# Performance work log

Hardware: AMD Instinct MI355X
Metric: run time of the kernel (lower is better)

Reference implementation:

```python
import jax, jax.numpy as jnp
import numpy as np

D_MODEL = 512
D_STATE = 16
D_CONV = 4
D_INNER = 1024  # expand_factor * d_model
HEADS = 8
D_K = D_MODEL // HEADS
EPS = 1e-5


def layer_norm(x, g, b):
    mu = jnp.mean(x, axis=-1, keepdims=True)
    var = jnp.var(x, axis=-1, keepdims=True)
    return (x - mu) / jnp.sqrt(var + EPS) * g + b


def silu(x):
    return x * jax.nn.sigmoid(x)


def setup_inputs() -> dict:
    key = jax.random.key(0)
    ks = jax.random.split(key, 20)
    s = 0.02

    def n(k, shape):
        return jax.random.normal(k, shape, jnp.float32) * s

    inp = {
        "x": jax.random.normal(ks[0], (8, 1024, D_MODEL), jnp.float32),
        # Mamba params (Linear weights stored as [in, out])
        "in_proj_w": n(ks[1], (D_MODEL, 2 * D_INNER)),
        "conv_w": n(ks[2], (D_INNER, D_CONV)),
        "conv_b": jnp.zeros((D_INNER,), jnp.float32),
        "x_proj_w": n(ks[3], (D_INNER, 2 * D_STATE)),
        "dt_proj_w": n(ks[4], (D_INNER, D_INNER)),
        "dt_proj_b": jnp.zeros((D_INNER,), jnp.float32),
        "A_log": jnp.log(jnp.arange(1, D_STATE + 1, dtype=jnp.float32)),
        "D": jnp.ones((D_INNER,), jnp.float32),
        "out_proj_w": n(ks[5], (D_INNER, D_MODEL)),
        # attention
        "wq_w": n(ks[6], (D_MODEL, D_MODEL)), "wq_b": jnp.zeros((D_MODEL,), jnp.float32),
        "wk_w": n(ks[7], (D_MODEL, D_MODEL)), "wk_b": jnp.zeros((D_MODEL,), jnp.float32),
        "wv_w": n(ks[8], (D_MODEL, D_MODEL)), "wv_b": jnp.zeros((D_MODEL,), jnp.float32),
        "wo_w": n(ks[9], (D_MODEL, D_MODEL)), "wo_b": jnp.zeros((D_MODEL,), jnp.float32),
        "attn_ln_g": jnp.ones((D_MODEL,), jnp.float32), "attn_ln_b": jnp.zeros((D_MODEL,), jnp.float32),
        # FFN
        "ffn_w1": n(ks[10], (D_MODEL, 4 * D_MODEL)), "ffn_b1": jnp.zeros((4 * D_MODEL,), jnp.float32),
        "ffn_w2": n(ks[11], (4 * D_MODEL, D_MODEL)), "ffn_b2": jnp.zeros((D_MODEL,), jnp.float32),
        # norms
        "norm1_g": jnp.ones((D_MODEL,), jnp.float32), "norm1_b": jnp.zeros((D_MODEL,), jnp.float32),
        "norm2_g": jnp.ones((D_MODEL,), jnp.float32), "norm2_b": jnp.zeros((D_MODEL,), jnp.float32),
        "norm3_g": jnp.ones((D_MODEL,), jnp.float32), "norm3_b": jnp.zeros((D_MODEL,), jnp.float32),
        # gate
        "gate_w": n(ks[12], (2 * D_MODEL, D_MODEL)), "gate_b": jnp.zeros((D_MODEL,), jnp.float32),
    }
    return inp


def selective_scan(u, delta, A, B, C, Dp):
    # u, delta: [b, L, d_inner]; B, C: [b, L, d_state]; A: [d_state]; Dp: [d_inner]
    def step(h, inp):
        u_i, d_i, B_i, C_i = inp
        dA = jnp.exp(d_i[:, None, :] * A[None, :, None])        # [b, S, di]
        h = h * dA + (d_i[:, None, :] * B_i[:, :, None]) * u_i[:, None, :]
        y_i = jnp.sum(h * C_i[:, :, None], axis=1)              # [b, di]
        return h, y_i

    b = u.shape[0]
    h0 = jnp.zeros((b, A.shape[0], u.shape[-1]), u.dtype)
    xs = (u.transpose(1, 0, 2), delta.transpose(1, 0, 2),
          B.transpose(1, 0, 2), C.transpose(1, 0, 2))
    _, ys = jax.lax.scan(step, h0, xs)                          # [L, b, di]
    y = ys.transpose(1, 0, 2)
    return y + u * Dp


def mamba(x, in_proj_w, conv_w, conv_b, x_proj_w, dt_proj_w, dt_proj_b, A_log, Dp, out_proj_w):
    L = x.shape[1]
    xr = x @ in_proj_w
    xm, res = jnp.split(xr, 2, axis=-1)                         # [b, L, di] each
    # causal depthwise conv1d: left pad d_conv-1
    xp = jnp.pad(xm, ((0, 0), (D_CONV - 1, 0), (0, 0)))
    xc = sum(conv_w[:, k] * xp[:, k:k + L, :] for k in range(D_CONV)) + conv_b
    xc = silu(xc)
    BC = xc @ x_proj_w
    B, C = jnp.split(BC, 2, axis=-1)                            # [b, L, d_state]
    delta = jax.nn.softplus(xc @ dt_proj_w + dt_proj_b)
    A = -jnp.exp(A_log)
    y = selective_scan(xc, delta, A, B, C, Dp)
    y = y * silu(res)
    return y @ out_proj_w


def attention(q_in, wq_w, wq_b, wk_w, wk_b, wv_w, wv_b, wo_w, wo_b, ln_g, ln_b):
    b, S, _ = q_in.shape
    Q = (q_in @ wq_w + wq_b).reshape(b, S, HEADS, D_K)
    K = (q_in @ wk_w + wk_b).reshape(b, S, HEADS, D_K)
    V = (q_in @ wv_w + wv_b).reshape(b, S, HEADS, D_K)
    scores = jnp.einsum('bqhd,bkhd->bhqk', Q, K) / np.sqrt(D_K).astype(np.float32)
    w = jax.nn.softmax(scores, axis=-1)
    out = jnp.einsum('bhqk,bkhd->bqhd', w, V).reshape(b, S, D_MODEL)
    out = out @ wo_w + wo_b
    return layer_norm(out + q_in, ln_g, ln_b), w


def reference(x, in_proj_w, conv_w, conv_b, x_proj_w, dt_proj_w, dt_proj_b, A_log, D,
              out_proj_w, wq_w, wq_b, wk_w, wk_b, wv_w, wv_b, wo_w, wo_b,
              attn_ln_g, attn_ln_b, ffn_w1, ffn_b1, ffn_w2, ffn_b2,
              norm1_g, norm1_b, norm2_g, norm2_b, norm3_g, norm3_b, gate_w, gate_b):
    mamba_out = mamba(layer_norm(x, norm1_g, norm1_b), in_proj_w, conv_w, conv_b,
                      x_proj_w, dt_proj_w, dt_proj_b, A_log, D, out_proj_w)
    x = x + mamba_out
    xn = layer_norm(x, norm2_g, norm2_b)
    attn_out, attn_w = attention(xn, wq_w, wq_b, wk_w, wk_b, wv_w, wv_b, wo_w, wo_b,
                                 attn_ln_g, attn_ln_b)
    x = x + attn_out
    combined = jnp.concatenate([mamba_out, attn_out], axis=-1)
    g = jax.nn.sigmoid(combined @ gate_w + gate_b)
    fused = g * mamba_out + (1.0 - g) * attn_out
    x = x + fused
    xn3 = layer_norm(x, norm3_g, norm3_b)
    ffn = jax.nn.gelu(xn3 @ ffn_w1 + ffn_b1) @ ffn_w2 + ffn_b2
    x = x + ffn
    return (x, attn_w)
```

## Files before the change

### kernel.cpp

```cpp
#include <hip/hip_runtime.h>

#define SEQL 1024
#define DMODEL 512
#define DINNER 1024
#define NROWS 8192
#define SEG 64
#define NSEG 16
#define LOG2E 1.4426950408889634f

typedef unsigned short u16;
typedef unsigned int u32;
using bf16x8 = __attribute__((ext_vector_type(8))) short;
using f32x4  = __attribute__((ext_vector_type(4))) float;
using u16x4  = __attribute__((ext_vector_type(4))) unsigned short;
using u16x8  = __attribute__((ext_vector_type(8))) unsigned short;

__device__ __forceinline__ float rcp_fast(float x){ return __builtin_amdgcn_rcpf(x); }
__device__ __forceinline__ float exp_fast(float x){ return __expf(x); }
#if __has_builtin(__builtin_amdgcn_exp2f)
__device__ __forceinline__ float exp2_fast(float x){ return __builtin_amdgcn_exp2f(x); }
#else
__device__ __forceinline__ float exp2_fast(float x){ return __expf(x*0.6931471805599453f); }
#endif
__device__ __forceinline__ float sigmoid_f(float x){ return rcp_fast(1.f+exp_fast(-x)); }
__device__ __forceinline__ float softplus_f(float x){ return fmaxf(x,0.f)+__logf(1.f+exp_fast(-fabsf(x))); }
__device__ __forceinline__ float gelu_f(float x){
  float u2 = 1.5957691216057308f*(x+0.044715f*x*x*x);
  float t = 1.f - 2.f*rcp_fast(1.f+exp_fast(u2));
  return 0.5f*x*(1.f+t);
}
__device__ __forceinline__ u16 f2bf(float f){
  u32 u = __builtin_bit_cast(u32, f);
  return (u16)((u + 0x7FFFu + ((u>>16)&1u)) >> 16);
}
__device__ __forceinline__ float bf2f(u16 h){
  return __builtin_bit_cast(float, (u32)h << 16);
}

typedef __attribute__((address_space(1))) const void g_void;
typedef __attribute__((address_space(3))) void l_void;
__device__ __forceinline__ void gl_lds16(const void* g, void* l){
  __builtin_amdgcn_global_load_lds((g_void*)g, (l_void*)l, 16, 0, 0);
}

struct WtDesc { const float* src; u16* dst; int K; int N; int t0; };
struct WtArgs { WtDesc d[11]; };

__global__ __launch_bounds__(256) void wt_k(WtArgs a)
{
  __shared__ float t[64][65];
  int bid = blockIdx.x;
  int i = 0;
  #pragma unroll
  for (int j=1;j<11;++j) if (bid >= a.d[j].t0) i = j;
  const float* src = a.d[i].src; u16* dst = a.d[i].dst;
  int K = a.d[i].K, N = a.d[i].N;
  int ntN = (N+63)>>6;
  int loc = bid - a.d[i].t0;
  int k0 = (loc / ntN)*64, n0 = (loc % ntN)*64;
  int tr = threadIdx.x>>4, tc = threadIdx.x&15;
  #pragma unroll
  for (int p=0;p<4;++p) {
    int r = p*16 + tr; int c = tc*4;
    if (n0 + c < N) {
      float4 v = *(const float4*)(src + (size_t)(k0+r)*N + n0 + c);
      t[r][c]=v.x; t[r][c+1]=v.y; t[r][c+2]=v.z; t[r][c+3]=v.w;
    }
  }
  __syncthreads();
  #pragma unroll
  for (int p=0;p<4;++p) {
    int n = p*16 + tr; int k = tc*4;
    if (n0 + n < N) {
      u16x4 o = { f2bf(t[k][n]), f2bf(t[k+1][n]), f2bf(t[k+2][n]), f2bf(t[k+3][n]) };
      *(u16x4*)(dst + (size_t)(n0+n)*K + k0 + k) = o;
    }
  }
}

__global__ __launch_bounds__(256) void pack3_k(const float* a, const float* b,
                                               const float* c, float* o)
{
  int t = blockIdx.x*256 + threadIdx.x;
  if (t < 512) o[t] = a[t];
  else if (t < 1024) o[t] = b[t-512];
  else if (t < 1536) o[t] = c[t-1024];
}

template<int AM>
__global__ __launch_bounds__(128) void ln_k(const void* av, const void* bv, float* resid,
                                            const float* g, const float* beta,
                                            float* outf, u16* outb)
{
  int row = blockIdx.x;
  int t = threadIdx.x;
  size_t off = (size_t)row*DMODEL + t*4;
  float4 v;
  if (AM==2) {
    u16x4 va = *(const u16x4*)((const u16*)av + off);
    v.x = bf2f(va[0]); v.y = bf2f(va[1]); v.z = bf2f(va[2]); v.w = bf2f(va[3]);
  } else {
    v = *(const float4*)((const float*)av + off);
  }
  if (AM==1) {
    u16x4 wb = *(const u16x4*)((const u16*)bv + off);
    v.x += bf2f(wb[0]); v.y += bf2f(wb[1]); v.z += bf2f(wb[2]); v.w += bf2f(wb[3]);
  } else if (AM==2) {
    float4 wb = *(const float4*)((const float*)bv + off);
    v.x += wb.x; v.y += wb.y; v.z += wb.z; v.w += wb.w;
  }
  if (resid) *(float4*)(resid + off) = v;
  float s = v.x+v.y+v.z+v.w;
  float q = v.x*v.x+v.y*v.y+v.z*v.z+v.w*v.w;
  #pragma unroll
  for (int o=1;o<64;o<<=1){ s += __shfl_xor(s,o); q += __shfl_xor(q,o); }
  __shared__ float ss[2], qq[2];
  int w = t>>6;
  if ((t&63)==0){ ss[w]=s; qq[w]=q; }
  __syncthreads();
  s = ss[0]+ss[1]; q = qq[0]+qq[1];
  float mean = s*(1.f/512.f);
  float var  = q*(1.f/512.f) - mean*mean;
  float rstd = rsqrtf(var + 1e-5f);
  int c = t*4;
  float4 gg = *(const float4*)(g+c);
  float4 bb = *(const float4*)(beta+c);
  float4 o4;
  o4.x = (v.x-mean)*rstd*gg.x + bb.x;
  o4.y = (v.y-mean)*rstd*gg.y + bb.y;
  o4.z = (v.z-mean)*rstd*gg.z + bb.z;
  o4.w = (v.w-mean)*rstd*gg.w + bb.w;
  if (outf) *(float4*)(outf + off) = o4;
  if (outb) {
    u16x4 ob = { f2bf(o4.x), f2bf(o4.y), f2bf(o4.z), f2bf(o4.w) };
    *(u16x4*)(outb + off) = ob;
  }
}

template<int EPI, int BMODE, int TN>
__global__ __launch_bounds__(256) void mm_k(
    const u16* Ab, int lda, const u16* Bb, int ldb,
    void* Cv, int ldc, int M, int N, int K,
    const float* bias, const float* p0, const float* p1, const float* p2,
    const u16* A2b, u16* aux)
{
  constexpr int NJ = TN/32;
  __shared__ u16 As[128][32];
  __shared__ u16 Bs[TN][32];
  const int tid = threadIdx.x;
  const int bx = blockIdx.x, by = blockIdx.y;
  float* Cf = (float*)Cv;
  u16* Cb = (u16*)Cv;
  const int row0 = by*128, col0 = bx*TN;
  const int sr = tid>>2, sc = tid&3;
  const int wv = tid>>6, lane = tid&63;
  const int wr = wv>>1, wc = wv&1;
  const int lr = lane&15, lk = (lane>>4)*8;
  const int lq = lane>>4;

  f32x4 acc[4][NJ];
  #pragma unroll
  for (int i=0;i<4;++i)
    #pragma unroll
    for (int j=0;j<NJ;++j)
      acc[i][j] = (f32x4){0.f,0.f,0.f,0.f};

  for (int k0=0; k0<K; k0+=32) {
    #pragma unroll
    for (int h=0; h<2; ++h) {
      int row = sr + h*64;
      const u16* src;
      if (BMODE==3) {
        int kk = k0 + sc*8;
        src = (kk < 512) ? Ab + (size_t)(row0+row)*512 + kk
                         : A2b + (size_t)(row0+row)*512 + (kk-512);
      } else {
        src = Ab + (size_t)(row0+row)*lda + k0 + sc*8;
      }
      gl_lds16(src, &As[row][sc*8]);
    }
    #pragma unroll
    for (int h=0; h<TN/64; ++h) {
      int rowb = sr + h*64;
      gl_lds16(Bb + (size_t)(col0+rowb)*ldb + k0 + sc*8, &Bs[rowb][sc*8]);
    }
    __syncthreads();
    bf16x8 fa[4], fb[NJ];
    #pragma unroll
    for (int i=0;i<4;++i) fa[i] = *(const bf16x8*)&As[wr*64 + i*16 + lr][lk];
    #pragma unroll
    for (int j=0;j<NJ;++j) fb[j] = *(const bf16x8*)&Bs[wc*(TN/2) + j*16 + lr][lk];
    #pragma unroll
    for (int i=0;i<4;++i)
      #pragma unroll
      for (int j=0;j<NJ;++j)
        acc[i][j] = __builtin_amdgcn_mfma_f32_16x16x32_bf16(fa[i], fb[j], acc[i][j], 0,0,0);
    __syncthreads();
  }

  #pragma unroll
  for (int i=0;i<4;++i) {
    #pragma unroll
    for (int j=0;j<NJ;++j) {
      int col = col0 + wc*(TN/2) + j*16 + lr;
      if (col >= N) continue;
      int rowbase = row0 + wr*64 + i*16 + lq*4;
      f32x4 v4 = acc[i][j];
      if (EPI==11 && col >= 1024) {
        int c2 = col-1024;
        int b2 = rowbase >> 10;
        int l2 = rowbase & 1023;
        float bv = bias[col];
        u16x4 pk = { f2bf(v4[0]+bv), f2bf(v4[1]+bv), f2bf(v4[2]+bv), f2bf(v4[3]+bv) };
        *(u16x4*)(aux + (size_t)b2*DMODEL*SEQL + (size_t)c2*SEQL + l2) = pk;
        continue;
      }
      #pragma unroll
      for (int r=0;r<4;++r) {
        int row = rowbase + r;
        size_t idx = (size_t)row*ldc + col;
        float v = v4[r];
        if (EPI==3) Cb[idx] = f2bf(gelu_f(v + bias[col]));
        else if (EPI==5) Cf[idx] = v + bias[col] + p0[idx];
        else if (EPI==6) {
          float g = sigmoid_f(v + bias[col]);
          float m  = bf2f(((const u16*)p0)[idx]);
          float at = bf2f(((const u16*)p1)[idx]);
          Cf[idx] = p2[idx] + at + g*m + (1.f-g)*at;
        }
        else if (EPI==7) Cb[idx] = f2bf(v);
        else if (EPI==8) Cb[idx] = f2bf(v + bias[col]);
        else if (EPI==11) {
          size_t i2 = (size_t)(col>>9)*4194304 + (size_t)row*512 + (col&511);
          Cb[i2] = f2bf(v + bias[col]);
        }
        else if (EPI==12) {
          if (col < 32) Cf[(size_t)row*32 + col] = v;
          else aux[(size_t)row*1024 + (col-32)] = f2bf(softplus_f(v + bias[col-32]));
        }
      }
    }
  }
}

__global__ __launch_bounds__(256) void attn_k(const u16* Qb, const u16* Kb,
                                              const u16* VTb, float* AW, u16* Hbb)
{
  __shared__ u16 Qs[32][72];
  __shared__ u16 Ps[32][520];
  __shared__ float smax[4][32];
  __shared__ float ssum[4][32];

  const int tid = threadIdx.x;
  const int w = tid>>6, lane = tid&63;
  const int qt = blockIdx.x, bh = blockIdx.y;
  const int b = bh>>3, h = bh&7;
  const int q0 = qt*32;
  const int lr = lane&15, lg = lane>>4;
  const int rw = lg*4;

  {
    int r = tid>>3, c = (tid&7)*8;
    const u16* src = Qb + ((size_t)(b*1024 + q0 + r))*512 + h*64 + c;
    *(uint4*)&Qs[r][c] = *(const uint4*)src;
  }
  __syncthreads();

  f32x4 acc0[16], acc1[16];
  #pragma unroll
  for (int j=0;j<16;++j){ acc0[j]=(f32x4){0.f,0.f,0.f,0.f}; acc1[j]=(f32x4){0.f,0.f,0.f,0.f}; }
  bf16x8 fa00 = *(const bf16x8*)&Qs[lr][lg*8];
  bf16x8 fa01 = *(const bf16x8*)&Qs[lr][32+lg*8];
  bf16x8 fa10 = *(const bf16x8*)&Qs[16+lr][lg*8];
  bf16x8 fa11 = *(const bf16x8*)&Qs[16+lr][32+lg*8];
  const u16* Kbase = Kb + ((size_t)(b*1024 + w*256))*512 + h*64;
  #pragma unroll
  for (int j=0;j<16;++j){
    const u16* krow = Kbase + (size_t)(j*16 + lr)*512 + lg*8;
    bf16x8 fb0 = *(const bf16x8*)krow;
    bf16x8 fb1 = *(const bf16x8*)(krow+32);
    acc0[j] = __builtin_amdgcn_mfma_f32_16x16x32_bf16(fa00, fb0, acc0[j], 0,0,0);
    acc0[j] = __builtin_amdgcn_mfma_f32_16x16x32_bf16(fa01, fb1, acc0[j], 0,0,0);
    acc1[j] = __builtin_amdgcn_mfma_f32_16x16x32_bf16(fa10, fb0, acc1[j], 0,0,0);
    acc1[j] = __builtin_amdgcn_mfma_f32_16x16x32_bf16(fa11, fb1, acc1[j], 0,0,0);
  }

  float mg0[4] = {-1e30f,-1e30f,-1e30f,-1e30f};
  float mg1[4] = {-1e30f,-1e30f,-1e30f,-1e30f};
  #pragma unroll
  for (int j=0;j<16;++j)
    #pragma unroll
    for (int r=0;r<4;++r){
      mg0[r]=fmaxf(mg0[r],acc0[j][r]);
      mg1[r]=fmaxf(mg1[r],acc1[j][r]);
    }
  #pragma unroll
  for (int o=1;o<16;o<<=1)
    #pragma unroll
    for (int r=0;r<4;++r){
      mg0[r]=fmaxf(mg0[r],__shfl_xor(mg0[r],o));
      mg1[r]=fmaxf(mg1[r],__shfl_xor(mg1[r],o));
    }
  if (lr==0){
    #pragma unroll
    for (int r=0;r<4;++r){ smax[w][rw+r]=mg0[r]; smax[w][16+rw+r]=mg1[r]; }
  }
  __syncthreads();
  #pragma unroll
  for (int r=0;r<4;++r){
    mg0[r] = fmaxf(fmaxf(smax[0][rw+r],smax[1][rw+r]),fmaxf(smax[2][rw+r],smax[3][rw+r]));
    mg1[r] = fmaxf(fmaxf(smax[0][16+rw+r],smax[1][16+rw+r]),fmaxf(smax[2][16+rw+r],smax[3][16+rw+r]));
  }
  const float cs = 0.125f*LOG2E;
  float sg0[4]={0.f,0.f,0.f,0.f}, sg1[4]={0.f,0.f,0.f,0.f};
  #pragma unroll
  for (int j=0;j<16;++j)
    #pragma unroll
    for (int r=0;r<4;++r){
      acc0[j][r]=exp2_fast((acc0[j][r]-mg0[r])*cs); sg0[r]+=acc0[j][r];
      acc1[j][r]=exp2_fast((acc1[j][r]-mg1[r])*cs); sg1[r]+=acc1[j][r];
    }
  #pragma unroll
  for (int o=1;o<16;o<<=1)
    #pragma unroll
    for (int r=0;r<4;++r){
      sg0[r]+=__shfl_xor(sg0[r],o);
      sg1[r]+=__shfl_xor(sg1[r],o);
    }
  if (lr==0){
    #pragma unroll
    for (int r=0;r<4;++r){ ssum[w][rw+r]=sg0[r]; ssum[w][16+rw+r]=sg1[r]; }
  }
  __syncthreads();
  float ig0[4], ig1[4];
  #pragma unroll
  for (int r=0;r<4;++r){
    ig0[r] = rcp_fast(ssum[0][rw+r]+ssum[1][rw+r]+ssum[2][rw+r]+ssum[3][rw+r]);
    ig1[r] = rcp_fast(ssum[0][16+rw+r]+ssum[1][16+rw+r]+ssum[2][16+rw+r]+ssum[3][16+rw+r]);
  }

  f32x4 av0 = (f32x4){0.f,0.f,0.f,0.f};
  f32x4 av1 = (f32x4){0.f,0.f,0.f,0.f};
  const u16* Vbase = VTb + (size_t)b*524288 + (size_t)(h*64 + w*16 + lr)*1024;

  #pragma unroll
  for (int half=0; half<2; ++half){
    if ((w>>1) == half) {
      #pragma unroll
      for (int j=0;j<16;++j){
        int col = (w&1)*256 + j*16 + lr;
        #pragma unroll
        for (int r=0;r<4;++r){
          Ps[rw+r][col]    = f2bf(acc0[j][r]*ig0[r]);
          Ps[16+rw+r][col] = f2bf(acc1[j][r]*ig1[r]);
        }
      }
    }
    __syncthreads();
    #pragma unroll
    for (int ks=0; ks<16; ++ks){
      bf16x8 fb  = *(const bf16x8*)(Vbase + half*512 + ks*32 + lg*8);
      bf16x8 pa0 = *(const bf16x8*)&Ps[lr][ks*32 + lg*8];
      bf16x8 pa1 = *(const bf16x8*)&Ps[16+lr][ks*32 + lg*8];
      av0 = __builtin_amdgcn_mfma_f32_16x16x32_bf16(pa0, fb, av0, 0,0,0);
      av1 = __builtin_amdgcn_mfma_f32_16x16x32_bf16(pa1, fb, av1, 0,0,0);
    }
    {
      float* awbase = AW + (size_t)bh*1048576 + (size_t)q0*1024 + half*512;
      int rowh = tid>>7;
      int c = (tid&127)*4;
      #pragma unroll
      for (int it=0; it<16; ++it) {
        int r = it*2 + rowh;
        u16x4 pv = *(const u16x4*)&Ps[r][c];
        float4 f0 = { bf2f(pv[0]), bf2f(pv[1]), bf2f(pv[2]), bf2f(pv[3]) };
        *(float4*)(awbase + (size_t)r*1024 + c) = f0;
      }
    }
    if (half==0) __syncthreads();
  }

  u16* ob = Hbb + ((size_t)(b*1024 + q0))*512 + h*64 + w*16 + lr;
  #pragma unroll
  for (int r=0;r<4;++r){
    ob[(size_t)(rw+r)*512]    = f2bf(av0[r]);
    ob[(size_t)(16+rw+r)*512] = f2bf(av1[r]);
  }
}

__global__ __launch_bounds__(256) void conv_k(const u16* xrb, const float* cw,
                                              const float* cb, u16* xcb)
{
  int t = blockIdx.x*256 + threadIdx.x;
  int d = (t & 255)*4;
  int row = t >> 8;
  int l = row & (SEQL-1);
  const u16* xmb = xrb + (size_t)(row - l)*2048 + d;
  float wv[4][4];
  #pragma unroll
  for (int dd=0; dd<4; ++dd){
    float4 w = *(const float4*)(cw + (size_t)(d+dd)*4);
    wv[dd][0]=w.x; wv[dd][1]=w.y; wv[dd][2]=w.z; wv[dd][3]=w.w;
  }
  float4 acc = *(const float4*)(cb + d);
  #pragma unroll
  for (int k=0;k<4;++k){
    int ls = l + k - 3;
    if (ls >= 0) {
      u16x4 xv = *(const u16x4*)(xmb + (size_t)ls*2048);
      acc.x += wv[0][k]*bf2f(xv[0]);
      acc.y += wv[1][k]*bf2f(xv[1]);
      acc.z += wv[2][k]*bf2f(xv[2]);
      acc.w += wv[3][k]*bf2f(xv[3]);
    }
  }
  float sx = acc.x*rcp_fast(1.f+exp_fast(-acc.x));
  float sy = acc.y*rcp_fast(1.f+exp_fast(-acc.y));
  float sz = acc.z*rcp_fast(1.f+exp_fast(-acc.z));
  float sw = acc.w*rcp_fast(1.f+exp_fast(-acc.w));
  size_t off = (size_t)row*DINNER + d;
  u16x4 ob = { f2bf(sx), f2bf(sy), f2bf(sz), f2bf(sw) };
  *(u16x4*)(xcb + off) = ob;
}

__global__ __launch_bounds__(256) void scan1_k(const u16* dtb, const u16* ub,
                                               const float* bc, const float* A_log,
                                               float* Pq)
{
  const int tid = threadIdx.x;
  const int d   = blockIdx.x*256 + tid;
  const int seg = blockIdx.y;
  const int b   = blockIdx.z;
  const int l0  = seg*SEG;

  __shared__ float BCs[SEG*32];
  {
    const float4* src = (const float4*)(bc + ((size_t)b*SEQL + l0)*32);
    float4* dst = (float4*)BCs;
    dst[tid]     = src[tid];
    dst[tid+256] = src[tid+256];
  }
  float As2[16];
  #pragma unroll
  for (int s=0;s<16;++s) As2[s] = -expf(A_log[s]) * LOG2E;
  __syncthreads();

  float h[16], P[16];
  #pragma unroll
  for (int s=0;s<16;++s){ h[s]=0.f; P[s]=1.f; }

  size_t base = ((size_t)b*SEQL + l0)*DINNER + d;
  const u16* pdt = dtb + base;
  const u16* pu  = ub  + base;

  u16 dpf[8], upf[8];
  #pragma unroll
  for (int j=0;j<8;++j){ dpf[j]=pdt[(size_t)j*DINNER]; upf[j]=pu[(size_t)j*DINNER]; }
  const u16* pdt_f = pdt + (size_t)8*DINNER;
  const u16* pu_f  = pu  + (size_t)8*DINNER;

  for (int l=0; l<SEG; l+=8) {
    bool pf = (l+8 < SEG);
    #pragma unroll
    for (int j=0;j<8;++j) {
      float dt = bf2f(dpf[j]), u = bf2f(upf[j]);
      if (pf) { dpf[j] = *pdt_f; upf[j] = *pu_f; }
      pdt_f += DINNER; pu_f += DINNER;
      float dtu = dt*u;
      const float* Bs = &BCs[(l+j)*32];
      #pragma unroll
      for (int s=0;s<16;++s) {
        float dA = exp2_fast(dt*As2[s]);
        P[s] *= dA;
        h[s] = fmaf(h[s], dA, dtu*Bs[s]);
      }
    }
  }
  float* out = Pq + (((size_t)b*NSEG + seg)*32)*1024 + d;
  #pragma unroll
  for (int s=0;s<16;++s) {
    out[(size_t)s*1024]      = P[s];
    out[(size_t)(16+s)*1024] = h[s];
  }
}

__global__ __launch_bounds__(256) void scan2_k(const u16* dtb, const u16* ub,
                                               const float* bc, const u16* xrb,
                                               const float* A_log, const float* Dp,
                                               const float* Pq, u16* yb)
{
  const int tid = threadIdx.x;
  const int d   = blockIdx.x*256 + tid;
  const int seg = blockIdx.y;
  const int b   = blockIdx.z;
  const int l0  = seg*SEG;

  __shared__ float BCs[SEG*32];
  {
    const float4* src = (const float4*)(bc + ((size_t)b*SEQL + l0)*32);
    float4* dst = (float4*)BCs;
    dst[tid]     = src[tid];
    dst[tid+256] = src[tid+256];
  }
  float As2[16];
  #pragma unroll
  for (int s=0;s<16;++s) As2[s] = -expf(A_log[s]) * LOG2E;
  float dcoef = Dp[d];
  __syncthreads();

  float h[16];
  #pragma unroll
  for (int s=0;s<16;++s) h[s]=0.f;

  const float* pp = Pq + ((size_t)b*NSEG)*32*1024 + d;
  for (int sg=0; sg<seg; ++sg) {
    const float* q = pp + (size_t)sg*32*1024;
    #pragma unroll
    for (int s=0;s<16;++s)
      h[s] = fmaf(h[s], q[(size_t)s*1024], q[(size_t)(16+s)*1024]);
  }

  size_t rbase = (size_t)b*SEQL + l0;
  const u16* pdt = dtb + rbase*DINNER + d;
  const u16* pu  = ub  + rbase*DINNER + d;
  const u16* pr  = xrb + rbase*2048 + 1024 + d;
  u16*       py  = yb  + rbase*DINNER + d;

  u16 dpf[8], upf[8], rpf[8];
  #pragma unroll
  for (int j=0;j<8;++j){
    dpf[j]=pdt[(size_t)j*DINNER]; upf[j]=pu[(size_t)j*DINNER]; rpf[j]=pr[(size_t)j*2048];
  }
  const u16* pdt_f = pdt + (size_t)8*DINNER;
  const u16* pu_f  = pu  + (size_t)8*DINNER;
  const u16* pr_f  = pr  + (size_t)8*2048;

  for (int l=0; l<SEG; l+=8) {
    bool pf = (l+8 < SEG);
    #pragma unroll
    for (int j=0;j<8;++j) {
      float dt = bf2f(dpf[j]), u = bf2f(upf[j]), rv = bf2f(rpf[j]);
      if (pf) { dpf[j] = *pdt_f; upf[j] = *pu_f; rpf[j] = *pr_f; }
      pdt_f += DINNER; pu_f += DINNER; pr_f += 2048;
      float dtu = dt*u;
      float acc = 0.f;
      const float* Bs = &BCs[(l+j)*32];
      #pragma unroll
      for (int s=0;s<16;++s) {
        float dA = exp2_fast(dt*As2[s]);
        h[s] = fmaf(h[s], dA, dtu*Bs[s]);
        acc  = fmaf(h[s], Bs[16+s], acc);
      }
      float y = fmaf(u, dcoef, acc);
      y *= rv * rcp_fast(1.f + exp2_fast(rv*(-LOG2E)));
      *py = f2bf(y);
      py += DINNER;
    }
  }
}

extern "C" void kernel_launch(void* const* d_in, const int* in_sizes, int n_in,
                              void* d_out, int out_size, void* d_ws, size_t ws_size,
                              hipStream_t stream)
{
  const float* x          = (const float*)d_in[0];
  const float* in_proj_w  = (const float*)d_in[1];
  const float* conv_w     = (const float*)d_in[2];
  const float* conv_b     = (const float*)d_in[3];
  const float* x_proj_w   = (const float*)d_in[4];
  const float* dt_proj_w  = (const float*)d_in[5];
  const float* dt_proj_b  = (const float*)d_in[6];
  const float* A_log      = (const float*)d_in[7];
  const float* Dvec       = (const float*)d_in[8];
  const float* out_proj_w = (const float*)d_in[9];
  const float* wq_w = (const float*)d_in[10]; const float* wq_b = (const float*)d_in[11];
  const float* wk_w = (const float*)d_in[12]; const float* wk_b = (const float*)d_in[13];
  const float* wv_w = (const float*)d_in[14]; const float* wv_b = (const float*)d_in[15];
  const float* wo_w = (const float*)d_in[16]; const float* wo_b = (const float*)d_in[17];
  const float* attn_ln_g = (const float*)d_in[18]; const float* attn_ln_b = (const float*)d_in[19];
  const float* ffn_w1 = (const float*)d_in[20]; const float* ffn_b1 = (const float*)d_in[21];
  const float* ffn_w2 = (const float*)d_in[22]; const float* ffn_b2 = (const float*)d_in[23];
  const float* norm1_g = (const float*)d_in[24]; const float* norm1_b = (const float*)d_in[25];
  const float* norm2_g = (const float*)d_in[26]; const float* norm2_b = (const float*)d_in[27];
  const float* norm3_g = (const float*)d_in[28]; const float* norm3_b = (const float*)d_in[29];
  const float* gate_w  = (const float*)d_in[30]; const float* gate_b  = (const float*)d_in[31];

  float* ws  = (float*)d_ws;
  float* BC   = ws;
  float* X1   = BC  + 262144;
  float* XN2  = X1  + 4194304;
  float* Pq   = XN2 + 4194304;
  u16* WT0 = (u16*)(Pq + 4194304);
  u16* XRb = WT0 + 6324224;
  u16* NB  = XRb + 16777216;
  u16* XCb = NB  + 4194304;
  u16* DTb = XCb + 8388608;
  u16* Yb  = DTb + 8388608;
  float* QKVB = (float*)(Yb + 8388608);

  u16* Qb   = XRb;
  u16* Kb   = XRb + 4194304;
  u16* VTb  = XRb + 8388608;
  u16* Hbb  = XRb + 12582912;
  u16* FHb  = XRb;
  u16* MBb  = XCb;
  u16* ATTb = XCb + 4194304;
  u16* WOUTb= DTb;

  u16* inprojT = WT0;
  u16* xprojT  = inprojT + 1048576;
  u16* dtT     = xprojT  + 32768;
  u16* outT    = dtT     + 1048576;
  u16* wqT     = outT    + 524288;
  u16* wkT     = wqT     + 262144;
  u16* wvT     = wkT     + 262144;
  u16* woT     = wvT     + 262144;
  u16* ffn1T   = woT     + 262144;
  u16* ffn2T   = ffn1T   + 1048576;
  u16* gateT   = ffn2T   + 1048576;

  float* XOUT = (float*)d_out;
  float* AW   = (float*)d_out + 4194304;

  const float* nulf = nullptr;
  u16* nulh = nullptr;

  WtArgs wa;
  wa.d[0]  = { in_proj_w, inprojT, 512, 2048, 0 };
  wa.d[1]  = { x_proj_w,  xprojT, 1024,   32, 256 };
  wa.d[2]  = { dt_proj_w, dtT,    1024, 1024, 272 };
  wa.d[3]  = { out_proj_w,outT,   1024,  512, 528 };
  wa.d[4]  = { wq_w,      wqT,     512,  512, 656 };
  wa.d[5]  = { wk_w,      wkT,     512,  512, 720 };
  wa.d[6]  = { wv_w,      wvT,     512,  512, 784 };
  wa.d[7]  = { wo_w,      woT,     512,  512, 848 };
  wa.d[8]  = { ffn_w1,    ffn1T,   512, 2048, 912 };
  wa.d[9]  = { ffn_w2,    ffn2T,  2048,  512, 1168 };
  wa.d[10] = { gate_w,    gateT,  1024,  512, 1424 };
  wt_k<<<1552, 256, 0, stream>>>(wa);
  pack3_k<<<6, 256, 0, stream>>>(wq_b, wk_b, wv_b, QKVB);

  ln_k<0><<<NROWS, 128, 0, stream>>>(x, nullptr, nullptr, norm1_g, norm1_b, nullptr, NB);
  mm_k<7,0,128><<<dim3(16,64), 256, 0, stream>>>(NB,512, inprojT,512, XRb,2048,
        NROWS,2048,512, nulf,nulf,nulf,nulf,nulh,nulh);
  conv_k<<<NROWS, 256, 0, stream>>>(XRb, conv_w, conv_b, XCb);
  mm_k<12,0,128><<<dim3(9,64), 256, 0, stream>>>(XCb,1024, xprojT,1024, BC,32,
        NROWS,1056,1024, dt_proj_b,nulf,nulf,nulf,nulh,DTb);
  scan1_k<<<dim3(4,NSEG-1,8), 256, 0, stream>>>(DTb, XCb, BC, A_log, Pq);
  scan2_k<<<dim3(4,NSEG,8),   256, 0, stream>>>(DTb, XCb, BC, XRb, A_log, Dvec, Pq, Yb);
  mm_k<7,0,64><<<dim3(8,64), 256, 0, stream>>>(Yb,1024, outT,1024, MBb,512,
        NROWS,512,1024, nulf,nulf,nulf,nulf,nulh,nulh);
  ln_k<1><<<NROWS, 128, 0, stream>>>(x, MBb, X1, norm2_g, norm2_b, XN2, NB);
  mm_k<11,0,128><<<dim3(12,64), 256, 0, stream>>>(NB,512, wqT,512, Qb,512,
        NROWS,1536,512, QKVB,nulf,nulf,nulf,nulh,VTb);
  attn_k<<<dim3(32,64), 256, 0, stream>>>(Qb, Kb, VTb, AW, Hbb);
  mm_k<8,0,64><<<dim3(8,64), 256, 0, stream>>>(Hbb,512, woT,512, WOUTb,512,
        NROWS,512,512, wo_b,nulf,nulf,nulf,nulh,nulh);
  ln_k<2><<<NROWS, 128, 0, stream>>>(WOUTb, XN2, nullptr, attn_ln_g, attn_ln_b, nullptr, ATTb);
  mm_k<6,3,64><<<dim3(8,64), 256, 0, stream>>>(MBb,512, gateT,1024, X1,512,
        NROWS,512,1024, gate_b, (const float*)MBb, (const float*)ATTb, X1, ATTb, nulh);
  ln_k<0><<<NROWS, 128, 0, stream>>>(X1, nullptr, nullptr, norm3_g, norm3_b, nullptr, NB);
  mm_k<3,0,128><<<dim3(16,64), 256, 0, stream>>>(NB,512, ffn1T,512, FHb,2048,
        NROWS,2048,512, ffn_b1,nulf,nulf,nulf,nulh,nulh);
  mm_k<5,0,64><<<dim3(8,64), 256, 0, stream>>>(FHb,2048, ffn2T,2048, XOUT,512,
        NROWS,512,2048, ffn_b2, X1,nulf,nulf,nulh,nulh);
}
```

Measured before the change: 617.7 us.

## Double-buffer GEMM LDS tiles, shrink M-tile for narrow GEMMs, one-wave-per-row layernorm

The GEMM kernel now double-buffers its A and B LDS tiles, issuing the next k-slice's global-to-LDS loads before computing on the current one, with one barrier per iteration. The M tile becomes a template parameter, and the N=512 GEMMs use 64x64 tiles with twice as many blocks to improve occupancy and wave count. LayerNorm processes one row per 64-lane wave with 8 elements per lane, which removes the shared-memory reduction and block barrier. Double buffering doubles LDS use per block, which may lower occupancy, and smaller tiles reduce data reuse.

After: 579.6 us. 6.2% less time.

```diff
diff --git a/kernel.cpp b/kernel.cpp
--- a/kernel.cpp
+++ b/kernel.cpp
@@ -88,86 +88,103 @@
 }
 
 template<int AM>
-__global__ __launch_bounds__(128) void ln_k(const void* av, const void* bv, float* resid,
+__global__ __launch_bounds__(256) void ln_k(const void* av, const void* bv, float* resid,
                                             const float* g, const float* beta,
                                             float* outf, u16* outb)
 {
-  int row = blockIdx.x;
-  int t = threadIdx.x;
-  size_t off = (size_t)row*DMODEL + t*4;
-  float4 v;
+  const int lane = threadIdx.x & 63;
+  const int row = (blockIdx.x<<2) + (threadIdx.x>>6);
+  size_t off = (size_t)row*DMODEL + lane*8;
+  float v[8];
   if (AM==2) {
-    u16x4 va = *(const u16x4*)((const u16*)av + off);
-    v.x = bf2f(va[0]); v.y = bf2f(va[1]); v.z = bf2f(va[2]); v.w = bf2f(va[3]);
+    u16x8 va = *(const u16x8*)((const u16*)av + off);
+    #pragma unroll
+    for (int i=0;i<8;++i) v[i] = bf2f(va[i]);
   } else {
-    v = *(const float4*)((const float*)av + off);
+    float4 a0 = *(const float4*)((const float*)av + off);
+    float4 a1 = *(const float4*)((const float*)av + off + 4);
+    v[0]=a0.x; v[1]=a0.y; v[2]=a0.z; v[3]=a0.w;
+    v[4]=a1.x; v[5]=a1.y; v[6]=a1.z; v[7]=a1.w;
   }
   if (AM==1) {
-    u16x4 wb = *(const u16x4*)((const u16*)bv + off);
-    v.x += bf2f(wb[0]); v.y += bf2f(wb[1]); v.z += bf2f(wb[2]); v.w += bf2f(wb[3]);
+    u16x8 wb = *(const u16x8*)((const u16*)bv + off);
+    #pragma unroll
+    for (int i=0;i<8;++i) v[i] += bf2f(wb[i]);
   } else if (AM==2) {
-    float4 wb = *(const float4*)((const float*)bv + off);
-    v.x += wb.x; v.y += wb.y; v.z += wb.z; v.w += wb.w;
-  }
-  if (resid) *(float4*)(resid + off) = v;
-  float s = v.x+v.y+v.z+v.w;
-  float q = v.x*v.x+v.y*v.y+v.z*v.z+v.w*v.w;
+    float4 b0 = *(const float4*)((const float*)bv + off);
+    float4 b1 = *(const float4*)((const float*)bv + off + 4);
+    v[0]+=b0.x; v[1]+=b0.y; v[2]+=b0.z; v[3]+=b0.w;
+    v[4]+=b1.x; v[5]+=b1.y; v[6]+=b1.z; v[7]+=b1.w;
+  }
+  if (resid) {
+    float4 r0 = {v[0],v[1],v[2],v[3]};
+    float4 r1 = {v[4],v[5],v[6],v[7]};
+    *(float4*)(resid + off) = r0;
+    *(float4*)(resid + off + 4) = r1;
+  }
+  float s=0.f, q=0.f;
+  #pragma unroll
+  for (int i=0;i<8;++i){ s += v[i]; q = fmaf(v[i], v[i], q); }
   #pragma unroll
   for (int o=1;o<64;o<<=1){ s += __shfl_xor(s,o); q += __shfl_xor(q,o); }
-  __shared__ float ss[2], qq[2];
-  int w = t>>6;
-  if ((t&63)==0){ ss[w]=s; qq[w]=q; }
-  __syncthreads();
-  s = ss[0]+ss[1]; q = qq[0]+qq[1];
   float mean = s*(1.f/512.f);
   float var  = q*(1.f/512.f) - mean*mean;
   float rstd = rsqrtf(var + 1e-5f);
-  int c = t*4;
-  float4 gg = *(const float4*)(g+c);
-  float4 bb = *(const float4*)(beta+c);
-  float4 o4;
-  o4.x = (v.x-mean)*rstd*gg.x + bb.x;
-  o4.y = (v.y-mean)*rstd*gg.y + bb.y;
-  o4.z = (v.z-mean)*rstd*gg.z + bb.z;
-  o4.w = (v.w-mean)*rstd*gg.w + bb.w;
-  if (outf) *(float4*)(outf + off) = o4;
+  int c = lane*8;
+  float4 g0 = *(const float4*)(g+c);
+  float4 g1 = *(const float4*)(g+c+4);
+  float4 b0 = *(const float4*)(beta+c);
+  float4 b1 = *(const float4*)(beta+c+4);
+  float gg[8] = {g0.x,g0.y,g0.z,g0.w,g1.x,g1.y,g1.z,g1.w};
+  float bb[8] = {b0.x,b0.y,b0.z,b0.w,b1.x,b1.y,b1.z,b1.w};
+  float o8[8];
+  #pragma unroll
+  for (int i=0;i<8;++i) o8[i] = (v[i]-mean)*rstd*gg[i] + bb[i];
+  if (outf) {
+    float4 f0 = {o8[0],o8[1],o8[2],o8[3]};
+    float4 f1 = {o8[4],o8[5],o8[6],o8[7]};
+    *(float4*)(outf + off) = f0;
+    *(float4*)(outf + off + 4) = f1;
+  }
   if (outb) {
-    u16x4 ob = { f2bf(o4.x), f2bf(o4.y), f2bf(o4.z), f2bf(o4.w) };
-    *(u16x4*)(outb + off) = ob;
-  }
-}
-
-template<int EPI, int BMODE, int TN>
+    u16x8 ob = { f2bf(o8[0]),f2bf(o8[1]),f2bf(o8[2]),f2bf(o8[3]),
+                 f2bf(o8[4]),f2bf(o8[5]),f2bf(o8[6]),f2bf(o8[7]) };
+    *(u16x8*)(outb + off) = ob;
+  }
+}
+
+template<int EPI, int BMODE, int TM, int TN>
 __global__ __launch_bounds__(256) void mm_k(
     const u16* Ab, int lda, const u16* Bb, int ldb,
     void* Cv, int ldc, int M, int N, int K,
     const float* bias, const float* p0, const float* p1, const float* p2,
     const u16* A2b, u16* aux)
 {
+  constexpr int NI = TM/32;
   constexpr int NJ = TN/32;
-  __shared__ u16 As[128][32];
-  __shared__ u16 Bs[TN][32];
+  __shared__ u16 As[2][TM][32];
+  __shared__ u16 Bs[2][TN][32];
   const int tid = threadIdx.x;
   const int bx = blockIdx.x, by = blockIdx.y;
   float* Cf = (float*)Cv;
   u16* Cb = (u16*)Cv;
-  const int row0 = by*128, col0 = bx*TN;
+  const int row0 = by*TM, col0 = bx*TN;
   const int sr = tid>>2, sc = tid&3;
   const int wv = tid>>6, lane = tid&63;
   const int wr = wv>>1, wc = wv&1;
   const int lr = lane&15, lk = (lane>>4)*8;
   const int lq = lane>>4;
 
-  f32x4 acc[4][NJ];
-  #pragma unroll
-  for (int i=0;i<4;++i)
+  f32x4 acc[NI][NJ];
+  #pragma unroll
+  for (int i=0;i<NI;++i)
     #pragma unroll
     for (int j=0;j<NJ;++j)
       acc[i][j] = (f32x4){0.f,0.f,0.f,0.f};
 
-  for (int k0=0; k0<K; k0+=32) {
-    #pragma unroll
-    for (int h=0; h<2; ++h) {
+  auto stage = [&](int buf, int k0){
+    #pragma unroll
+    for (int h=0; h<TM/64; ++h) {
       int row = sr + h*64;
       const u16* src;
       if (BMODE==3) {
@@ -177,21 +194,28 @@
       } else {
         src = Ab + (size_t)(row0+row)*lda + k0 + sc*8;
       }
-      gl_lds16(src, &As[row][sc*8]);
+      gl_lds16(src, &As[buf][row][sc*8]);
     }
     #pragma unroll
     for (int h=0; h<TN/64; ++h) {
       int rowb = sr + h*64;
-      gl_lds16(Bb + (size_t)(col0+rowb)*ldb + k0 + sc*8, &Bs[rowb][sc*8]);
-    }
-    __syncthreads();
-    bf16x8 fa[4], fb[NJ];
-    #pragma unroll
-    for (int i=0;i<4;++i) fa[i] = *(const bf16x8*)&As[wr*64 + i*16 + lr][lk];
-    #pragma unroll
-    for (int j=0;j<NJ;++j) fb[j] = *(const bf16x8*)&Bs[wc*(TN/2) + j*16 + lr][lk];
-    #pragma unroll
-    for (int i=0;i<4;++i)
+      gl_lds16(Bb + (size_t)(col0+rowb)*ldb + k0 + sc*8, &Bs[buf][rowb][sc*8]);
+    }
+  };
+
+  const int nt = K/32;
+  stage(0, 0);
+  __syncthreads();
+  for (int t=0; t<nt; ++t) {
+    int buf = t&1;
+    if (t+1 < nt) stage(buf^1, (t+1)*32);
+    bf16x8 fa[NI], fb[NJ];
+    #pragma unroll
+    for (int i=0;i<NI;++i) fa[i] = *(const bf16x8*)&As[buf][wr*(TM/2) + i*16 + lr][lk];
+    #pragma unroll
+    for (int j=0;j<NJ;++j) fb[j] = *(const bf16x8*)&Bs[buf][wc*(TN/2) + j*16 + lr][lk];
+    #pragma unroll
+    for (int i=0;i<NI;++i)
       #pragma unroll
       for (int j=0;j<NJ;++j)
         acc[i][j] = __builtin_amdgcn_mfma_f32_16x16x32_bf16(fa[i], fb[j], acc[i][j], 0,0,0);
@@ -199,12 +223,12 @@
   }
 
   #pragma unroll
-  for (int i=0;i<4;++i) {
+  for (int i=0;i<NI;++i) {
     #pragma unroll
     for (int j=0;j<NJ;++j) {
       int col = col0 + wc*(TN/2) + j*16 + lr;
       if (col >= N) continue;
-      int rowbase = row0 + wr*64 + i*16 + lq*4;
+      int rowbase = row0 + wr*(TM/2) + i*16 + lq*4;
       f32x4 v4 = acc[i][j];
       if (EPI==11 && col >= 1024) {
         int c2 = col-1024;
@@ -640,28 +664,28 @@
   wt_k<<<1552, 256, 0, stream>>>(wa);
   pack3_k<<<6, 256, 0, stream>>>(wq_b, wk_b, wv_b, QKVB);
 
-  ln_k<0><<<NROWS, 128, 0, stream>>>(x, nullptr, nullptr, norm1_g, norm1_b, nullptr, NB);
-  mm_k<7,0,128><<<dim3(16,64), 256, 0, stream>>>(NB,512, inprojT,512, XRb,2048,
+  ln_k<0><<<2048, 256, 0, stream>>>(x, nullptr, nullptr, norm1_g, norm1_b, nullptr, NB);
+  mm_k<7,0,128,128><<<dim3(16,64), 256, 0, stream>>>(NB,512, inprojT,512, XRb,2048,
         NROWS,2048,512, nulf,nulf,nulf,nulf,nulh,nulh);
   conv_k<<<NROWS, 256, 0, stream>>>(XRb, conv_w, conv_b, XCb);
-  mm_k<12,0,128><<<dim3(9,64), 256, 0, stream>>>(XCb,1024, xprojT,1024, BC,32,
+  mm_k<12,0,128,128><<<dim3(9,64), 256, 0, stream>>>(XCb,1024, xprojT,1024, BC,32,
         NROWS,1056,1024, dt_proj_b,nulf,nulf,nulf,nulh,DTb);
   scan1_k<<<dim3(4,NSEG-1,8), 256, 0, stream>>>(DTb, XCb, BC, A_log, Pq);
   scan2_k<<<dim3(4,NSEG,8),   256, 0, stream>>>(DTb, XCb, BC, XRb, A_log, Dvec, Pq, Yb);
-  mm_k<7,0,64><<<dim3(8,64), 256, 0, stream>>>(Yb,1024, outT,1024, MBb,512,
+  mm_k<7,0,64,64><<<dim3(8,128), 256, 0, stream>>>(Yb,1024, outT,1024, MBb,512,
         NROWS,512,1024, nulf,nulf,nulf,nulf,nulh,nulh);
-  ln_k<1><<<NROWS, 128, 0, stream>>>(x, MBb, X1, norm2_g, norm2_b, XN2, NB);
-  mm_k<11,0,128><<<dim3(12,64), 256, 0, stream>>>(NB,512, wqT,512, Qb,512,
+  ln_k<1><<<2048, 256, 0, stream>>>(x, MBb, X1, norm2_g, norm2_b, XN2, NB);
+  mm_k<11,0,128,128><<<dim3(12,64), 256, 0, stream>>>(NB,512, wqT,512, Qb,512,
         NROWS,1536,512, QKVB,nulf,nulf,nulf,nulh,VTb);
   attn_k<<<dim3(32,64), 256, 0, stream>>>(Qb, Kb, VTb, AW, Hbb);
-  mm_k<8,0,64><<<dim3(8,64), 256, 0, stream>>>(Hbb,512, woT,512, WOUTb,512,
+  mm_k<8,0,64,64><<<dim3(8,128), 256, 0, stream>>>(Hbb,512, woT,512, WOUTb,512,
         NROWS,512,512, wo_b,nulf,nulf,nulf,nulh,nulh);
-  ln_k<2><<<NROWS, 128, 0, stream>>>(WOUTb, XN2, nullptr, attn_ln_g, attn_ln_b, nullptr, ATTb);
-  mm_k<6,3,64><<<dim3(8,64), 256, 0, stream>>>(MBb,512, gateT,1024, X1,512,
+  ln_k<2><<<2048, 256, 0, stream>>>(WOUTb, XN2, nullptr, attn_ln_g, attn_ln_b, nullptr, ATTb);
+  mm_k<6,3,64,64><<<dim3(8,128), 256, 0, stream>>>(MBb,512, gateT,1024, X1,512,
         NROWS,512,1024, gate_b, (const float*)MBb, (const float*)ATTb, X1, ATTb, nulh);
-  ln_k<0><<<NROWS, 128, 0, stream>>>(X1, nullptr, nullptr, norm3_g, norm3_b, nullptr, NB);
-  mm_k<3,0,128><<<dim3(16,64), 256, 0, stream>>>(NB,512, ffn1T,512, FHb,2048,
+  ln_k<0><<<2048, 256, 0, stream>>>(X1, nullptr, nullptr, norm3_g, norm3_b, nullptr, NB);
+  mm_k<3,0,128,128><<<dim3(16,64), 256, 0, stream>>>(NB,512, ffn1T,512, FHb,2048,
         NROWS,2048,512, ffn_b1,nulf,nulf,nulf,nulh,nulh);
-  mm_k<5,0,64><<<dim3(8,64), 256, 0, stream>>>(FHb,2048, ffn2T,2048, XOUT,512,
+  mm_k<5,0,64,64><<<dim3(8,128), 256, 0, stream>>>(FHb,2048, ffn2T,2048, XOUT,512,
         NROWS,512,2048, ffn_b2, X1,nulf,nulf,nulh,nulh);
 }
```
